# Kernel optimization log

Hardware: AMD Instinct MI355X
Metric: run time of the kernel (lower is better)

Reference implementation:

```python
import jax, jax.numpy as jnp
import numpy as np

N_FLUID = 16384
N_BND = 2048
SUPPORT = float(np.sqrt(16.0 / (np.pi * N_FLUID)))  # ~16 neighbors avg
NB = 8  # basis functions per axis (n = m = 8)
NM = NB * NB
LAYERS = [32, 64, 64, 2]
F_IN = 8
B_IN = 8


def _radius(queries, points, r):
    """numpy brute-force (chunked) radius search; rows = query idx, cols = point idx."""
    r2 = np.float32(r * r)
    pn = (points ** 2).sum(-1)
    qi_all, pj_all = [], []
    for s in range(0, queries.shape[0], 4096):
        q = queries[s:s + 4096]
        d2 = (q ** 2).sum(-1)[:, None] + pn[None, :] - 2.0 * (q @ points.T)
        qi, pj = np.nonzero(d2 < r2)
        qi_all.append(qi + s)
        pj_all.append(pj)
    return (np.concatenate(qi_all).astype(np.int32),
            np.concatenate(pj_all).astype(np.int32))


def setup_inputs() -> dict:
    rng = np.random.default_rng(0)
    fluid_pos = rng.random((N_FLUID, 2)).astype(np.float32)
    # boundary particles along the perimeter of the unit square
    t = np.linspace(0.0, 4.0, N_BND, endpoint=False).astype(np.float32)
    side = np.floor(t).astype(np.int64)
    frac = t - side
    bx = np.where(side == 0, frac, np.where(side == 1, 1.0, np.where(side == 2, 1.0 - frac, 0.0)))
    by = np.where(side == 0, 0.0, np.where(side == 1, frac, np.where(side == 2, 1.0, 1.0 - frac)))
    bnd_pos = np.stack([bx, by], -1).astype(np.float32)

    # fluid-fluid radius graph (centerIgnore: drop self edges)
    fi, fj = _radius(fluid_pos, fluid_pos, SUPPORT)
    keep = fi != fj
    f_tgt, f_src = fi[keep], fj[keep]
    # fluid(query) - boundary(source) radius graph
    b_tgt, b_src = _radius(fluid_pos, bnd_pos, SUPPORT)

    def conv_w(k, cin, cout):
        return (0.05 * rng.standard_normal((NM, cin, cout))).astype(np.float32)

    def lin_w(cin, cout):
        s = np.sqrt(6.0 / (cin + cout))
        return rng.uniform(-s, s, (cin, cout)).astype(np.float32)

    d = {
        'fluid_pos': jnp.asarray(fluid_pos),
        'bnd_pos': jnp.asarray(bnd_pos),
        'fluid_feat': jnp.asarray(rng.standard_normal((N_FLUID, F_IN)).astype(np.float32)),
        'bnd_feat': jnp.asarray(rng.standard_normal((N_BND, B_IN)).astype(np.float32)),
        'f_tgt': jnp.asarray(f_tgt), 'f_src': jnp.asarray(f_src),
        'b_tgt': jnp.asarray(b_tgt), 'b_src': jnp.asarray(b_src),
        # convs: c0 fluid->fluid (F_IN->32), c1 boundary->fluid (B_IN->32),
        #        c2 (96->64), c3 (64->64), c4 (64->2)
        'Wc0': jnp.asarray(conv_w(0, F_IN, 32)), 'bc0': jnp.zeros((32,), jnp.float32),
        'Wc1': jnp.asarray(conv_w(1, B_IN, 32)), 'bc1': jnp.zeros((32,), jnp.float32),
        'Wc2': jnp.asarray(conv_w(2, 96, 64)), 'bc2': jnp.zeros((64,), jnp.float32),
        'Wc3': jnp.asarray(conv_w(3, 64, 64)), 'bc3': jnp.zeros((64,), jnp.float32),
        'Wc4': jnp.asarray(conv_w(4, 64, 2)), 'bc4': jnp.zeros((2,), jnp.float32),
        # dense branch: l0 (F_IN->32), l1 (96->64), l2 (64->64), l3 (64->2)
        'Wl0': jnp.asarray(lin_w(F_IN, 32)), 'bl0': jnp.zeros((32,), jnp.float32),
        'Wl1': jnp.asarray(lin_w(96, 64)), 'bl1': jnp.zeros((64,), jnp.float32),
        'Wl2': jnp.asarray(lin_w(64, 64)), 'bl2': jnp.zeros((64,), jnp.float32),
        'Wl3': jnp.asarray(lin_w(64, 2)), 'bl3': jnp.zeros((2,), jnp.float32),
    }
    return d


def _hat(x, n):
    # linear 'hat' RBF basis on centers in [-1, 1]
    c = jnp.linspace(-1.0, 1.0, n, dtype=x.dtype)
    return jnp.maximum(0.0, 1.0 - jnp.abs(x[:, None] - c[None, :]) * ((n - 1) / 2.0))


def _polar(d):
    # polar coordinate mapping of normalized displacement d in [-1,1]^2
    r = jnp.sqrt(jnp.sum(d * d, -1) + 1e-12)
    theta = jnp.arctan2(d[:, 1], d[:, 0])
    return jnp.clip(jnp.stack([2.0 * r - 1.0, theta / jnp.pi], -1), -1.0, 1.0)


def _rbf_conv(x_src_nodes, src, tgt, disp, W, b, num_tgt):
    m = _polar(disp)                                   # [E,2]
    bx = _hat(m[:, 0], NB)                             # [E,n]
    by = _hat(m[:, 1], NB)                             # [E,m]
    basis = (bx[:, :, None] * by[:, None, :]).reshape(-1, NM)  # [E,nm]
    xs = x_src_nodes[src]                              # [E,cin]
    acc0 = jnp.zeros((xs.shape[0], W.shape[-1]), xs.dtype)

    def body(acc, wb):
        Wk, bk = wb
        return acc + bk[:, None] * (xs @ Wk), None

    msg, _ = jax.lax.scan(body, acc0, (W, basis.T))    # sum_k basis_k * (xs @ W_k)
    return jax.ops.segment_sum(msg, tgt, num_segments=num_tgt) + b


def reference(fluid_pos, bnd_pos, fluid_feat, bnd_feat, f_tgt, f_src, b_tgt, b_src,
              Wc0, bc0, Wc1, bc1, Wc2, bc2, Wc3, bc3, Wc4, bc4,
              Wl0, bl0, Wl1, bl1, Wl2, bl2, Wl3, bl3):
    N = fluid_feat.shape[0]
    fdisp = jnp.clip(-(fluid_pos[f_src] - fluid_pos[f_tgt]) / SUPPORT, -1.0, 1.0)
    bdisp = jnp.clip((bnd_pos[b_src] - fluid_pos[b_tgt]) / SUPPORT, -1.0, 1.0)

    lin = fluid_feat @ Wl0 + bl0
    fconv = _rbf_conv(fluid_feat, f_src, f_tgt, fdisp, Wc0, bc0, N)
    bconv = _rbf_conv(bnd_feat, b_src, b_tgt, bdisp, Wc1, bc1, N)
    ans = jnp.concatenate([lin, fconv, bconv], axis=-1)  # [N, 96]

    blocks = [(Wc2, bc2, Wl1, bl1, False), (Wc3, bc3, Wl2, bl2, True), (Wc4, bc4, Wl3, bl3, False)]
    for Wc, bc, Wl, bl, residual in blocks:
        a = jax.nn.relu(ans)
        c = _rbf_conv(a, f_src, f_tgt, fdisp, Wc, bc, N)
        dns = a @ Wl + bl
        ans = c + dns + ans if residual else c + dns
    return ans / 128.0
```

## Files before the change

kernel.cpp:

```cpp
#include <hip/hip_runtime.h>
#include <math.h>
#include <stdint.h>

#define NFL   16384
#define NCC   55
#define PADQ  128

struct EdgeData { int src; int ixiy; float fx; float fy; };

typedef _Float16 half8 __attribute__((ext_vector_type(8)));
typedef __attribute__((ext_vector_type(4))) float f32x4;

__device__ __forceinline__ float frelu(float x){ return x > 0.f ? x : 0.f; }
__device__ __forceinline__ unsigned short f2bf(float f){
    unsigned int u = __float_as_uint(f);
    unsigned int r = (u + 0x7FFFu + ((u >> 16) & 1u)) >> 16;
    return (unsigned short)r;
}

__device__ __forceinline__ EdgeData make_edge(const float* qpos, const float* ppos,
                                              int t, int s, float support, float sgn)
{
    float dx = sgn * (ppos[2*s]   - qpos[2*t])   / support;
    float dy = sgn * (ppos[2*s+1] - qpos[2*t+1]) / support;
    dx = fminf(1.f, fmaxf(-1.f, dx));
    dy = fminf(1.f, fmaxf(-1.f, dy));
    float r  = sqrtf(dx*dx + dy*dy + 1e-12f);
    float th = atan2f(dy, dx);
    float m0 = fminf(1.f, fmaxf(-1.f, 2.f*r - 1.f));
    float m1 = fminf(1.f, fmaxf(-1.f, th * 0.3183098861837907f));
    float u = (m0 + 1.f) * 3.5f;
    float v = (m1 + 1.f) * 3.5f;
    int ix = (int)u; if (ix > 6) ix = 6;
    int iy = (int)v; if (iy > 6) iy = 6;
    EdgeData ed;
    ed.src  = s;
    ed.ixiy = ix*8 + iy;
    ed.fx   = u - (float)ix;
    ed.fy   = v - (float)iy;
    return ed;
}

__global__ __launch_bounds__(256)
void setup_k(const float* __restrict__ fluid_pos, const float* __restrict__ bnd_pos,
             const int* __restrict__ f_tgt, const int* __restrict__ f_src, int nEf,
             const int* __restrict__ b_tgt, const int* __restrict__ b_src, int nEb,
             float support,
             EdgeData* __restrict__ edF, EdgeData* __restrict__ edB,
             int* __restrict__ hpart,
             int* __restrict__ rowptrF, int* __restrict__ rowptrB,
             const float* __restrict__ Wc2, const float* __restrict__ Wc3,
             const float* __restrict__ Wc0,
             _Float16* __restrict__ wt2, _Float16* __restrict__ wt3,
             unsigned short* __restrict__ wb0,
             int nA, int nB, int nC)
{
    __shared__ int lc[64];
    __shared__ _Float16 T[64][98];
    int b = blockIdx.x, tid = threadIdx.x;
    if (b < nA){
        if (tid < 64) lc[tid] = 0;
        __syncthreads();
        int e = b*256 + tid;
        if (e < nEf){
            EdgeData d = make_edge(fluid_pos, fluid_pos, f_tgt[e], f_src[e], support, -1.f);
            edF[e] = d;
            atomicAdd(&lc[d.ixiy], 1);
        }
        __syncthreads();
        if (tid < 64) hpart[b*64 + tid] = lc[tid];
    } else if (b < nA + nB){
        int e = (b - nA)*256 + tid;
        if (e < nEb)
            edB[e] = make_edge(fluid_pos, bnd_pos, b_tgt[e], b_src[e], support, 1.f);
    } else if (b < nA + nB + nC){
        int t = (b - nA - nB)*256 + tid;
        if (t > NFL) return;
        if (t == NFL){ rowptrF[NFL] = nEf; return; }
        int lo = 0, hi = nEf;
        while (lo < hi){ int mid = (lo + hi) >> 1; if (f_tgt[mid] < t) lo = mid + 1; else hi = mid; }
        rowptrF[t] = lo;
    } else if (b < nA + nB + 2*nC){
        int t = (b - nA - nB - nC)*256 + tid;
        if (t > NFL) return;
        if (t == NFL){ rowptrB[NFL] = nEb; return; }
        int lo = 0, hi = nEb;
        while (lo < hi){ int mid = (lo + hi) >> 1; if (b_tgt[mid] < t) lo = mid + 1; else hi = mid; }
        rowptrB[t] = lo;
    } else {
        int wb = b - (nA + nB + 2*nC);
        if (wb < 64){
            const float* s = Wc2 + (size_t)wb * 96 * 64;
            for (int i = tid; i < 96*64; i += 256){ int k = i/64, c = i - k*64; T[c][k] = (_Float16)s[i]; }
            __syncthreads();
            _Float16* d = wt2 + (size_t)wb * 64 * 96;
            for (int i = tid; i < 96*64; i += 256){ int c = i/96, k = i - c*96; d[i] = T[c][k]; }
        } else if (wb < 128){
            int cell = wb - 64;
            const float* s = Wc3 + (size_t)cell * 64 * 64;
            for (int i = tid; i < 64*64; i += 256){ int k = i/64, c = i - k*64; T[c][k] = (_Float16)s[i]; }
            __syncthreads();
            _Float16* d = wt3 + (size_t)cell * 64 * 64;
            for (int i = tid; i < 64*64; i += 256){ int c = i/64, k = i - c*64; d[i] = T[c][k]; }
        } else {
            for (int i = tid; i < 64*8*32; i += 256) wb0[i] = f2bf(Wc0[i]);
        }
    }
}

__global__ __launch_bounds__(1024)
void scan_pad_k(const int* __restrict__ hpart, int nHB,
                int* __restrict__ cellOff,
                int* __restrict__ gcursor, int4* __restrict__ entries)
{
    __shared__ int red[16][64];
    __shared__ int cntS[64];
    __shared__ int offS[NCC+1];
    int tid = threadIdx.x;
    int c = tid & 63, j = tid >> 6;

    int s0 = 0, s1 = 0, s2 = 0, s3 = 0;
    int b = j;
    for (; b + 48 < nHB; b += 64){
        s0 += hpart[(b     )*64 + c];
        s1 += hpart[(b + 16)*64 + c];
        s2 += hpart[(b + 32)*64 + c];
        s3 += hpart[(b + 48)*64 + c];
    }
    for (; b < nHB; b += 16) s0 += hpart[b*64 + c];
    red[j][c] = s0 + s1 + s2 + s3;
    __syncthreads();

    if (tid < 64){
        int s = 0;
#pragma unroll
        for (int k = 0; k < 16; ++k) s += red[k][tid];
        cntS[tid] = s;
        gcursor[tid] = 0;
    }
    __syncthreads();
    if (tid == 0){
        int acc = 0;
        for (int k = 0; k < NCC; ++k){
            offS[k] = acc;
            acc += ((cntS[k] + PADQ - 1) / PADQ) * PADQ;
        }
        offS[NCC] = acc;
        for (int k = 0; k <= NCC; ++k) cellOff[k] = offS[k];
    }
    __syncthreads();
    for (int k = 0; k < NCC; ++k){
        int base = offS[k] + cntS[k];
        int pads = (offS[k+1] - offS[k]) - cntS[k];
        for (int i = tid; i < pads; i += 1024)
            entries[base + i] = make_int4(0, -1, 0, 0);
    }
}

__global__ void scatter_k(const EdgeData* __restrict__ ed, int nE,
                          const int* __restrict__ cellOff,
                          int* __restrict__ gcursor,
                          int4* __restrict__ entries)
{
    __shared__ int lc[64], base[64];
    int tid = threadIdx.x;
    if (tid < 64) lc[tid] = 0;
    __syncthreads();
    int e = blockIdx.x * blockDim.x + tid;
    bool ok = e < nE;
    EdgeData d; int k = 0, r = 0;
    if (ok){ d = ed[e]; k = d.ixiy; r = atomicAdd(&lc[k], 1); }
    __syncthreads();
    if (tid < 64 && lc[tid] > 0) base[tid] = atomicAdd(&gcursor[tid], lc[tid]);
    __syncthreads();
    if (ok){
        int slot = cellOff[k] + base[k] + r;
        entries[slot] = make_int4(d.src, e, __float_as_int(d.fx), __float_as_int(d.fy));
    }
}

template<int CIN>
__global__ __launch_bounds__(256)
void conv_mfma_k(const _Float16* __restrict__ xh,
                 const int4* __restrict__ entries,
                 const int* __restrict__ cellOff,
                 const _Float16* __restrict__ wt,
                 _Float16* __restrict__ msg)
{
    constexpr int COUT = 64;
    constexpr int XROW = CIN*2 + 16;
    constexpr int C16  = CIN*2/16;
    constexpr int NK   = CIN/32;
    constexpr int NCH  = PADQ/64;

    __shared__ unsigned char XL[64 * XROW];
    __shared__ _Float16 MT[64][68];
    __shared__ float BW[4][64];
    __shared__ int   SRC[64];
    __shared__ int   EID[64];

    int total = cellOff[NCC];
    int nwg = gridDim.x, bid = blockIdx.x;
    int q = nwg >> 3, r = nwg & 7;
    int xcd = bid & 7, idx = bid >> 3;
    int swz = (xcd < r ? xcd*(q+1) : r*(q+1) + (xcd - r)*q) + idx;
    int pb = swz * PADQ;
    if (pb >= total) return;
    int tid = threadIdx.x;

    int lo_ = 0, hi_ = NCC;
    while (hi_ - lo_ > 1){ int mid = (lo_ + hi_) >> 1; if (cellOff[mid] <= pb) lo_ = mid; else hi_ = mid; }
    const int cell = lo_;
    const int kc[4] = { cell, cell+1, cell+8, cell+9 };

    const int lane = tid & 63, wv = tid >> 6;
    const int lr = lane & 15, lg = lane >> 4;
    const int cb = wv * 16;

    const _Float16* wbase = wt + (size_t)(cb + lr) * CIN + lg * 8;
    half8 bfr[4][NK];
#pragma unroll
    for (int cr = 0; cr < 4; ++cr)
#pragma unroll
        for (int kk = 0; kk < NK; ++kk)
            bfr[cr][kk] = *(const half8*)(wbase + (size_t)kc[cr]*(COUT*CIN) + kk*32);

    for (int ch = 0; ch < NCH; ++ch){
        int p0 = pb + ch * 64;

        if (tid < 64){
            int4 en = entries[p0 + tid];
            bool ok = en.y >= 0;
            float fx = __int_as_float(en.z), fy = __int_as_float(en.w);
            BW[0][tid] = ok ? (1.f-fx)*(1.f-fy) : 0.f;
            BW[1][tid] = ok ? (1.f-fx)*fy       : 0.f;
            BW[2][tid] = ok ? fx*(1.f-fy)       : 0.f;
            BW[3][tid] = ok ? fx*fy             : 0.f;
            SRC[tid] = en.x;
            EID[tid] = en.y;
        }
        __syncthreads();
        for (int i = tid; i < 64*C16; i += 256){
            int e = i / C16, c = i - e*C16;
            const uint4* sp = (const uint4*)(xh + (size_t)SRC[e]*CIN) + c;
            *(uint4*)(&XL[e*XROW + 16*c]) = *sp;
        }
        __syncthreads();

        f32x4 acc[4][4];
#pragma unroll
        for (int cr = 0; cr < 4; ++cr)
#pragma unroll
            for (int ae = 0; ae < 4; ++ae)
                acc[cr][ae] = (f32x4)0.f;

#pragma unroll
        for (int kk = 0; kk < NK; ++kk){
            half8 a[4];
#pragma unroll
            for (int ae = 0; ae < 4; ++ae)
                a[ae] = *(const half8*)(&XL[(16*ae + lr)*XROW + kk*64 + lg*16]);
#pragma unroll
            for (int cr = 0; cr < 4; ++cr)
#pragma unroll
                for (int ae = 0; ae < 4; ++ae)
                    acc[cr][ae] = __builtin_amdgcn_mfma_f32_16x16x32_f16(a[ae], bfr[cr][kk], acc[cr][ae], 0, 0, 0);
        }

#pragma unroll
        for (int ae = 0; ae < 4; ++ae){
#pragma unroll
            for (int r2 = 0; r2 < 4; ++r2){
                int E = 16*ae + lg*4 + r2;
                float v = BW[0][E]*acc[0][ae][r2] + BW[1][E]*acc[1][ae][r2]
                        + BW[2][E]*acc[2][ae][r2] + BW[3][E]*acc[3][ae][r2];
                MT[E][cb + lr] = (_Float16)v;
            }
        }
        __syncthreads();

#pragma unroll
        for (int p = 0; p < 2; ++p){
            int f = tid + p*256;
            int e = f >> 3, j = f & 7;
            int eid = EID[e];
            if (eid >= 0)
                *(uint4*)(msg + (size_t)eid*COUT + j*8) = *(const uint4*)(&MT[e][j*8]);
        }
        __syncthreads();
    }
}

template<int CIN, int COUT, int TILE_E, bool RELU>
__global__ __launch_bounds__(128)
void conv_cell_k(const float* __restrict__ x,
                 const int4* __restrict__ entries,
                 const int* __restrict__ cellOff,
                 const unsigned short* __restrict__ Wbf,
                 _Float16* __restrict__ msg)
{
    constexpr int TEP = TILE_E + 4;
    constexpr int EG  = TILE_E / 4;
    constexpr int CG  = COUT / 8;
    static_assert(EG * CG == 128, "tile/thread mismatch");
    constexpr int C4  = CIN / 4;

    __shared__ float XT[CIN][TEP];
    __shared__ unsigned short WLc[4][CIN][COUT];
    __shared__ int4 EN[TILE_E];

    int total = cellOff[NCC];
    int p0 = blockIdx.x * TILE_E;
    if (p0 >= total) return;
    int tid = threadIdx.x;

    int lo = 0, hi = NCC;
    while (hi - lo > 1){ int mid = (lo + hi) >> 1; if (cellOff[mid] <= p0) lo = mid; else hi = mid; }
    const int cell = lo;

    for (int i = tid; i < TILE_E; i += 128) EN[i] = entries[p0 + i];

    const int kc[4] = { cell, cell + 1, cell + 8, cell + 9 };
#pragma unroll
    for (int c = 0; c < 4; ++c){
        const uint4* s = (const uint4*)(Wbf + (size_t)kc[c] * (CIN * COUT));
        uint4* dlds = (uint4*)(&WLc[c][0][0]);
        for (int i = tid; i < CIN * COUT / 8; i += 128) dlds[i] = s[i];
    }
    __syncthreads();

    for (int i = tid; i < TILE_E * C4; i += 128){
        int e  = i / C4;
        int c4 = i - e * C4;
        int4 en = EN[e];
        float4 v = make_float4(0.f, 0.f, 0.f, 0.f);
        if (en.y >= 0){
            v = *(const float4*)(x + (size_t)en.x * CIN + 4 * c4);
            if (RELU){ v.x = frelu(v.x); v.y = frelu(v.y); v.z = frelu(v.z); v.w = frelu(v.w); }
        }
        XT[4*c4+0][e] = v.x;
        XT[4*c4+1][e] = v.y;
        XT[4*c4+2][e] = v.z;
        XT[4*c4+3][e] = v.w;
    }
    __syncthreads();

    const int egrp = tid % EG;
    const int cgrp = tid / EG;
    const int e0 = egrp * 4;

    float fx[4], fy[4];
    int eid[4];
#pragma unroll
    for (int j = 0; j < 4; ++j){
        int4 en = EN[e0 + j];
        fx[j] = __int_as_float(en.z);
        fy[j] = __int_as_float(en.w);
        eid[j] = en.y;
    }

    float accT[4][8];
#pragma unroll
    for (int j = 0; j < 4; ++j)
#pragma unroll
        for (int c = 0; c < 8; ++c) accT[j][c] = 0.f;

#pragma unroll
    for (int cr = 0; cr < 4; ++cr){
        float accC[4][8];
#pragma unroll
        for (int j = 0; j < 4; ++j)
#pragma unroll
            for (int c = 0; c < 8; ++c) accC[j][c] = 0.f;

#pragma unroll
        for (int ci = 0; ci < CIN; ++ci){
            float4 xv = *(const float4*)&XT[ci][e0];
            uint4 wp = *(const uint4*)&WLc[cr][ci][cgrp * 8];
            float wf0 = __uint_as_float(wp.x << 16);
            float wf1 = __uint_as_float(wp.x & 0xFFFF0000u);
            float wf2 = __uint_as_float(wp.y << 16);
            float wf3 = __uint_as_float(wp.y & 0xFFFF0000u);
            float wf4 = __uint_as_float(wp.z << 16);
            float wf5 = __uint_as_float(wp.z & 0xFFFF0000u);
            float wf6 = __uint_as_float(wp.w << 16);
            float wf7 = __uint_as_float(wp.w & 0xFFFF0000u);
            const float xe[4] = { xv.x, xv.y, xv.z, xv.w };
#pragma unroll
            for (int j = 0; j < 4; ++j){
                accC[j][0] += xe[j] * wf0;
                accC[j][1] += xe[j] * wf1;
                accC[j][2] += xe[j] * wf2;
                accC[j][3] += xe[j] * wf3;
                accC[j][4] += xe[j] * wf4;
                accC[j][5] += xe[j] * wf5;
                accC[j][6] += xe[j] * wf6;
                accC[j][7] += xe[j] * wf7;
            }
        }
#pragma unroll
        for (int j = 0; j < 4; ++j){
            float wc = (cr == 0) ? (1.f - fx[j]) * (1.f - fy[j]) :
                       (cr == 1) ? (1.f - fx[j]) * fy[j] :
                       (cr == 2) ? fx[j] * (1.f - fy[j]) :
                                   fx[j] * fy[j];
#pragma unroll
            for (int c = 0; c < 8; ++c) accT[j][c] += wc * accC[j][c];
        }
    }

#pragma unroll
    for (int j = 0; j < 4; ++j){
        if (eid[j] < 0) continue;
        half8 hv;
#pragma unroll
        for (int c = 0; c < 8; ++c) hv[c] = (_Float16)accT[j][c];
        *(half8*)(msg + (size_t)eid[j] * COUT + cgrp * 8) = hv;
    }
}

__global__ __launch_bounds__(128)
void conv2_msg_k(const _Float16* __restrict__ xh,
                 const int4* __restrict__ entries,
                 const int* __restrict__ cellOff,
                 const float* __restrict__ Wc,
                 float* __restrict__ msg2)
{
    __shared__ float WLf[4][64][2];
    int total = cellOff[NCC];
    int p0 = blockIdx.x * 128;
    if (p0 >= total) return;
    int tid = threadIdx.x;

    int lo = 0, hi = NCC;
    while (hi - lo > 1){ int mid = (lo + hi) >> 1; if (cellOff[mid] <= p0) lo = mid; else hi = mid; }
    const int cell = lo;
    const int kc[4] = { cell, cell + 1, cell + 8, cell + 9 };
#pragma unroll
    for (int c = 0; c < 4; ++c)
        ((float*)&WLf[c][0][0])[tid] = Wc[(size_t)kc[c] * 128 + tid];
    __syncthreads();

    int4 en = entries[p0 + tid];
    if (en.y < 0) return;
    float fx = __int_as_float(en.z), fy = __int_as_float(en.w);
    const _Float16* xp = xh + (size_t)en.x * 64;

    float a[4][2] = {{0.f,0.f},{0.f,0.f},{0.f,0.f},{0.f,0.f}};
#pragma unroll
    for (int ci = 0; ci < 64; ci += 8){
        half8 v = *(const half8*)(xp + ci);
#pragma unroll
        for (int j = 0; j < 8; ++j){
            float xe = (float)v[j];
#pragma unroll
            for (int cr = 0; cr < 4; ++cr){
                a[cr][0] += xe * WLf[cr][ci+j][0];
                a[cr][1] += xe * WLf[cr][ci+j][1];
            }
        }
    }
    float w0 = (1.f-fx)*(1.f-fy), w1 = (1.f-fx)*fy, w2 = fx*(1.f-fy), w3 = fx*fy;
    float m0 = w0*a[0][0] + w1*a[1][0] + w2*a[2][0] + w3*a[3][0];
    float m1 = w0*a[0][1] + w1*a[1][1] + w2*a[2][1] + w3*a[3][1];
    *(float2*)(msg2 + (size_t)en.y * 2) = make_float2(m0, m1);
}

__global__ __launch_bounds__(256)
void final_combine_k(const _Float16* __restrict__ xh,
                     const float* __restrict__ Wl3, const float* __restrict__ bl3,
                     const float* __restrict__ bc4,
                     const float* __restrict__ msg2,
                     const int* __restrict__ rowptr,
                     float* __restrict__ out)
{
    __shared__ float WS[128];
    int tid = threadIdx.x;
    if (tid < 128) WS[tid] = Wl3[tid];
    __syncthreads();

    int t = blockIdx.x * blockDim.x + tid;
    if (t >= NFL) return;
    int eb = rowptr[t], ee = rowptr[t+1];

    float a0 = bc4[0] + bl3[0];
    float a1 = bc4[1] + bl3[1];
    const _Float16* pr = xh + (size_t)t * 64;
#pragma unroll
    for (int ci = 0; ci < 64; ci += 8){
        half8 v = *(const half8*)(pr + ci);
#pragma unroll
        for (int j = 0; j < 8; ++j){
            float xe = (float)v[j];
            a0 += xe * WS[(ci+j)*2];
            a1 += xe * WS[(ci+j)*2 + 1];
        }
    }
    for (int e = eb; e < ee; ++e){
        float2 m = *(const float2*)(msg2 + (size_t)e * 2);
        a0 += m.x; a1 += m.y;
    }
    out[(size_t)t*2]     = a0 * (1.0f/128.0f);
    out[(size_t)t*2 + 1] = a1 * (1.0f/128.0f);
}

__global__ __launch_bounds__(256)
void combine0_k(const float* __restrict__ feat,
                const float* __restrict__ bnd_feat,
                const float* __restrict__ Wl0, const float* __restrict__ bl0,
                const float* __restrict__ bc0,
                const float* __restrict__ Wc1, const float* __restrict__ bc1,
                const EdgeData* __restrict__ edB,
                const int* __restrict__ rowptrB,
                const _Float16* __restrict__ msg,
                const int* __restrict__ rowptrF,
                float* __restrict__ ansA,
                _Float16* __restrict__ xbA)
{
    int t = blockIdx.x * (blockDim.x >> 6) + (threadIdx.x >> 6);
    if (t >= NFL) return;
    int lane = threadIdx.x & 63;

    if (lane < 32){
        float a = bl0[lane];
#pragma unroll
        for (int ci = 0; ci < 8; ++ci)
            a += feat[t*8 + ci] * Wl0[ci*32 + lane];
        ansA[(size_t)t*96 + lane] = a;
        xbA[(size_t)t*96 + lane]  = (_Float16)frelu(a);

        float b = bc1[lane];
        int eb = rowptrB[t], ee = rowptrB[t+1];
        for (int e = eb; e < ee; ++e){
            EdgeData d = edB[e];
            const float* xp = bnd_feat + (size_t)d.src * 8;
            const float* wp = Wc1 + (size_t)d.ixiy * 256 + lane;
            float t00 = 0.f, t01 = 0.f, t10 = 0.f, t11 = 0.f;
#pragma unroll
            for (int ci = 0; ci < 8; ++ci){
                float xv = xp[ci];
                t00 += xv * wp[ci*32];
                t01 += xv * wp[ci*32 + 256];
                t10 += xv * wp[ci*32 + 2048];
                t11 += xv * wp[ci*32 + 2304];
            }
            float wx1 = d.fx, wy1 = d.fy;
            float wx0 = 1.f - wx1, wy0 = 1.f - wy1;
            b += (wx0*wy0)*t00 + (wx0*wy1)*t01 + (wx1*wy0)*t10 + (wx1*wy1)*t11;
        }
        ansA[(size_t)t*96 + 64 + lane] = b;
        xbA[(size_t)t*96 + 64 + lane]  = (_Float16)frelu(b);
    } else {
        int c = lane - 32;
        float a = bc0[c];
        int eb = rowptrF[t], ee = rowptrF[t+1];
        for (int e = eb; e < ee; ++e)
            a += (float)msg[(size_t)e*32 + c];
        ansA[(size_t)t*96 + 32 + c] = a;
        xbA[(size_t)t*96 + 32 + c]  = (_Float16)frelu(a);
    }
}

template<int CIN, bool RESID, bool WRITE_XB>
__global__ __launch_bounds__(256)
void combine12_k(const float* __restrict__ yprev,
                 const _Float16* __restrict__ xprev,
                 const float* __restrict__ Wl, const float* __restrict__ bl,
                 const float* __restrict__ bc,
                 const _Float16* __restrict__ msg,
                 const int* __restrict__ rowptr,
                 float* __restrict__ y,
                 _Float16* __restrict__ xbnext)
{
    int t = blockIdx.x * (blockDim.x >> 6) + (threadIdx.x >> 6);
    if (t >= NFL) return;
    int lane = threadIdx.x & 63;
    int eb = rowptr[t], ee = rowptr[t+1];

    const _Float16* pr = xprev + (size_t)t * CIN;
    float acc = bc[lane] + bl[lane];
#pragma unroll 8
    for (int ci = 0; ci < CIN; ++ci)
        acc += (float)pr[ci] * Wl[ci*64 + lane];
    if (RESID) acc += yprev[(size_t)t*64 + lane];

    for (int e = eb; e < ee; ++e)
        acc += (float)msg[(size_t)e*64 + lane];
    y[(size_t)t*64 + lane] = acc;

    if (WRITE_XB)
        xbnext[(size_t)t*64 + lane] = (_Float16)frelu(acc);
}

extern "C" void kernel_launch(void* const* d_in, const int* in_sizes, int n_in,
                              void* d_out, int out_size, void* d_ws, size_t ws_size,
                              hipStream_t stream)
{
    const float* fluid_pos  = (const float*)d_in[0];
    const float* bnd_pos    = (const float*)d_in[1];
    const float* fluid_feat = (const float*)d_in[2];
    const float* bnd_feat   = (const float*)d_in[3];
    const int*   f_tgt      = (const int*)  d_in[4];
    const int*   f_src      = (const int*)  d_in[5];
    const int*   b_tgt      = (const int*)  d_in[6];
    const int*   b_src      = (const int*)  d_in[7];
    const float* Wc0 = (const float*)d_in[8];  const float* bc0 = (const float*)d_in[9];
    const float* Wc1 = (const float*)d_in[10]; const float* bc1 = (const float*)d_in[11];
    const float* Wc2 = (const float*)d_in[12]; const float* bc2 = (const float*)d_in[13];
    const float* Wc3 = (const float*)d_in[14]; const float* bc3 = (const float*)d_in[15];
    const float* Wc4 = (const float*)d_in[16]; const float* bc4 = (const float*)d_in[17];
    const float* Wl0 = (const float*)d_in[18]; const float* bl0 = (const float*)d_in[19];
    const float* Wl1 = (const float*)d_in[20]; const float* bl1 = (const float*)d_in[21];
    const float* Wl2 = (const float*)d_in[22]; const float* bl2 = (const float*)d_in[23];
    const float* Wl3 = (const float*)d_in[24]; const float* bl3 = (const float*)d_in[25];

    int nEf = in_sizes[4];
    int nEb = in_sizes[6];
    int entPadMax = nEf + NCC * PADQ;
    float support = (float)sqrt(16.0 / (M_PI * 16384.0));

    int nA = (nEf + 255)/256, nB = (nEb + 255)/256, nC = (NFL + 256)/256;

    char* w = (char*)d_ws;
    auto alloc = [&](size_t bytes){ char* r = w; w += (bytes + 255) & ~(size_t)255; return r; };
    EdgeData* edF      = (EdgeData*)alloc((size_t)nEf * sizeof(EdgeData));
    EdgeData* edB      = (EdgeData*)alloc((size_t)nEb * sizeof(EdgeData));
    int*      hpart    = (int*)     alloc((size_t)nA * 64 * sizeof(int));
    int*      cellOff  = (int*)     alloc(64 * sizeof(int));
    int*      gcursor  = (int*)     alloc(64 * sizeof(int));
    int*      rowptrF  = (int*)     alloc((NFL+1) * sizeof(int));
    int*      rowptrB  = (int*)     alloc((NFL+1) * sizeof(int));
    int4*     entries  = (int4*)    alloc((size_t)entPadMax * sizeof(int4));
    unsigned short* wb0 = (unsigned short*)alloc((size_t)64*8*32 * 2);
    _Float16* wt2      = (_Float16*)alloc((size_t)64*64*96 * 2);
    _Float16* wt3      = (_Float16*)alloc((size_t)64*64*64 * 2);
    _Float16* xbA      = (_Float16*)alloc((size_t)NFL*96 * 2);
    _Float16* xb1      = (_Float16*)alloc((size_t)NFL*64 * 2);
    _Float16* xb2      = (_Float16*)alloc((size_t)NFL*64 * 2);
    float*    ansA     = (float*)   alloc((size_t)NFL * 96 * sizeof(float));
    float*    y1       = (float*)   alloc((size_t)NFL * 64 * sizeof(float));
    float*    y2       = (float*)   alloc((size_t)NFL * 64 * sizeof(float));
    _Float16* msg      = (_Float16*)alloc((size_t)nEf * 64 * 2);
    float*    msg2     = (float*)   alloc((size_t)nEf * 2 * sizeof(float));

    setup_k<<<nA + nB + 2*nC + 129, 256, 0, stream>>>(fluid_pos, bnd_pos,
                                                      f_tgt, f_src, nEf,
                                                      b_tgt, b_src, nEb, support,
                                                      edF, edB, hpart, rowptrF, rowptrB,
                                                      Wc2, Wc3, Wc0, wt2, wt3, wb0,
                                                      nA, nB, nC);
    scan_pad_k<<<1, 1024, 0, stream>>>(hpart, nA, cellOff, gcursor, entries);
    scatter_k<<<nA, 256, 0, stream>>>(edF, nEf, cellOff, gcursor, entries);

    int gridM = (entPadMax + PADQ - 1) / PADQ;
    int gridC = (entPadMax + 127) / 128;
    dim3 tgrid(NFL/4);

    conv_cell_k<8,32,128,false><<<gridC, 128, 0, stream>>>(fluid_feat, entries, cellOff, wb0, msg);
    combine0_k<<<tgrid, 256, 0, stream>>>(fluid_feat, bnd_feat, Wl0, bl0, bc0,
                                          Wc1, bc1, edB, rowptrB,
                                          msg, rowptrF, ansA, xbA);

    conv_mfma_k<96><<<gridM, 256, 0, stream>>>(xbA, entries, cellOff, wt2, msg);
    combine12_k<96,false,true><<<tgrid, 256, 0, stream>>>(nullptr, xbA, Wl1, bl1, bc2, msg, rowptrF, y1, xb1);

    conv_mfma_k<64><<<gridM, 256, 0, stream>>>(xb1, entries, cellOff, wt3, msg);
    combine12_k<64,true,true><<<tgrid, 256, 0, stream>>>(y1, xb1, Wl2, bl2, bc3, msg, rowptrF, y2, xb2);

    conv2_msg_k<<<gridC, 128, 0, stream>>>(xb2, entries, cellOff, Wc4, msg2);
    final_combine_k<<<(NFL+255)/256, 256, 0, stream>>>(xb2, Wl3, bl3, bc4, msg2, rowptrF, (float*)d_out);
}
```

Baseline: 247.5 us.

## Fuse first fluid conv into combine0 with per-target gather from LDS weights

Removes the separate cell-tiled conv kernel for the first fluid-fluid convolution (CIN=8, COUT=32) and its fp16 message buffer round-trip. combine0 now loads the full bf16 weight bank (64x8x32) into shared memory per block and computes each target's messages directly by gathering source features per edge with bilinear weights. This saves a launch and the message write/read, but every block of 4 targets reloads 32KB of weights into LDS and does scalar per-edge math in a CSR loop.

```diff
diff --git a/kernel.cpp b/kernel.cpp
--- a/kernel.cpp
+++ b/kernel.cpp
@@ -16,6 +16,9 @@
     unsigned int u = __float_as_uint(f);
     unsigned int r = (u + 0x7FFFu + ((u >> 16) & 1u)) >> 16;
     return (unsigned short)r;
+}
+__device__ __forceinline__ float bf2f(unsigned short u){
+    return __uint_as_float(((unsigned int)u) << 16);
 }
 
 __device__ __forceinline__ EdgeData make_edge(const float* qpos, const float* ppos,
@@ -291,134 +294,6 @@
     }
 }
 
-template<int CIN, int COUT, int TILE_E, bool RELU>
-__global__ __launch_bounds__(128)
-void conv_cell_k(const float* __restrict__ x,
-                 const int4* __restrict__ entries,
-                 const int* __restrict__ cellOff,
-                 const unsigned short* __restrict__ Wbf,
-                 _Float16* __restrict__ msg)
-{
-    constexpr int TEP = TILE_E + 4;
-    constexpr int EG  = TILE_E / 4;
-    constexpr int CG  = COUT / 8;
-    static_assert(EG * CG == 128, "tile/thread mismatch");
-    constexpr int C4  = CIN / 4;
-
-    __shared__ float XT[CIN][TEP];
-    __shared__ unsigned short WLc[4][CIN][COUT];
-    __shared__ int4 EN[TILE_E];
-
-    int total = cellOff[NCC];
-    int p0 = blockIdx.x * TILE_E;
-    if (p0 >= total) return;
-    int tid = threadIdx.x;
-
-    int lo = 0, hi = NCC;
-    while (hi - lo > 1){ int mid = (lo + hi) >> 1; if (cellOff[mid] <= p0) lo = mid; else hi = mid; }
-    const int cell = lo;
-
-    for (int i = tid; i < TILE_E; i += 128) EN[i] = entries[p0 + i];
-
-    const int kc[4] = { cell, cell + 1, cell + 8, cell + 9 };
-#pragma unroll
-    for (int c = 0; c < 4; ++c){
-        const uint4* s = (const uint4*)(Wbf + (size_t)kc[c] * (CIN * COUT));
-        uint4* dlds = (uint4*)(&WLc[c][0][0]);
-        for (int i = tid; i < CIN * COUT / 8; i += 128) dlds[i] = s[i];
-    }
-    __syncthreads();
-
-    for (int i = tid; i < TILE_E * C4; i += 128){
-        int e  = i / C4;
-        int c4 = i - e * C4;
-        int4 en = EN[e];
-        float4 v = make_float4(0.f, 0.f, 0.f, 0.f);
-        if (en.y >= 0){
-            v = *(const float4*)(x + (size_t)en.x * CIN + 4 * c4);
-            if (RELU){ v.x = frelu(v.x); v.y = frelu(v.y); v.z = frelu(v.z); v.w = frelu(v.w); }
-        }
-        XT[4*c4+0][e] = v.x;
-        XT[4*c4+1][e] = v.y;
-        XT[4*c4+2][e] = v.z;
-        XT[4*c4+3][e] = v.w;
-    }
-    __syncthreads();
-
-    const int egrp = tid % EG;
-    const int cgrp = tid / EG;
-    const int e0 = egrp * 4;
-
-    float fx[4], fy[4];
-    int eid[4];
-#pragma unroll
-    for (int j = 0; j < 4; ++j){
-        int4 en = EN[e0 + j];
-        fx[j] = __int_as_float(en.z);
-        fy[j] = __int_as_float(en.w);
-        eid[j] = en.y;
-    }
-
-    float accT[4][8];
-#pragma unroll
-    for (int j = 0; j < 4; ++j)
-#pragma unroll
-        for (int c = 0; c < 8; ++c) accT[j][c] = 0.f;
-
-#pragma unroll
-    for (int cr = 0; cr < 4; ++cr){
-        float accC[4][8];
-#pragma unroll
-        for (int j = 0; j < 4; ++j)
-#pragma unroll
-            for (int c = 0; c < 8; ++c) accC[j][c] = 0.f;
-
-#pragma unroll
-        for (int ci = 0; ci < CIN; ++ci){
-            float4 xv = *(const float4*)&XT[ci][e0];
-            uint4 wp = *(const uint4*)&WLc[cr][ci][cgrp * 8];
-            float wf0 = __uint_as_float(wp.x << 16);
-            float wf1 = __uint_as_float(wp.x & 0xFFFF0000u);
-            float wf2 = __uint_as_float(wp.y << 16);
-            float wf3 = __uint_as_float(wp.y & 0xFFFF0000u);
-            float wf4 = __uint_as_float(wp.z << 16);
-            float wf5 = __uint_as_float(wp.z & 0xFFFF0000u);
-            float wf6 = __uint_as_float(wp.w << 16);
-            float wf7 = __uint_as_float(wp.w & 0xFFFF0000u);
-            const float xe[4] = { xv.x, xv.y, xv.z, xv.w };
-#pragma unroll
-            for (int j = 0; j < 4; ++j){
-                accC[j][0] += xe[j] * wf0;
-                accC[j][1] += xe[j] * wf1;
-                accC[j][2] += xe[j] * wf2;
-                accC[j][3] += xe[j] * wf3;
-                accC[j][4] += xe[j] * wf4;
-                accC[j][5] += xe[j] * wf5;
-                accC[j][6] += xe[j] * wf6;
-                accC[j][7] += xe[j] * wf7;
-            }
-        }
-#pragma unroll
-        for (int j = 0; j < 4; ++j){
-            float wc = (cr == 0) ? (1.f - fx[j]) * (1.f - fy[j]) :
-                       (cr == 1) ? (1.f - fx[j]) * fy[j] :
-                       (cr == 2) ? fx[j] * (1.f - fy[j]) :
-                                   fx[j] * fy[j];
-#pragma unroll
-            for (int c = 0; c < 8; ++c) accT[j][c] += wc * accC[j][c];
-        }
-    }
-
-#pragma unroll
-    for (int j = 0; j < 4; ++j){
-        if (eid[j] < 0) continue;
-        half8 hv;
-#pragma unroll
-        for (int c = 0; c < 8; ++c) hv[c] = (_Float16)accT[j][c];
-        *(half8*)(msg + (size_t)eid[j] * COUT + cgrp * 8) = hv;
-    }
-}
-
 __global__ __launch_bounds__(128)
 void conv2_msg_k(const _Float16* __restrict__ xh,
                  const int4* __restrict__ entries,
@@ -512,14 +387,21 @@
                 const float* __restrict__ Wc1, const float* __restrict__ bc1,
                 const EdgeData* __restrict__ edB,
                 const int* __restrict__ rowptrB,
-                const _Float16* __restrict__ msg,
+                const EdgeData* __restrict__ edF,
                 const int* __restrict__ rowptrF,
+                const unsigned short* __restrict__ wb0,
                 float* __restrict__ ansA,
                 _Float16* __restrict__ xbA)
 {
-    int t = blockIdx.x * (blockDim.x >> 6) + (threadIdx.x >> 6);
+    __shared__ unsigned short WL0[64*8*32];
+    int tid = threadIdx.x;
+    for (int i = tid; i < 64*8*32/8; i += 256)
+        ((uint4*)WL0)[i] = ((const uint4*)wb0)[i];
+    __syncthreads();
+
+    int t = blockIdx.x * 4 + (tid >> 6);
     if (t >= NFL) return;
-    int lane = threadIdx.x & 63;
+    int lane = tid & 63;
 
     if (lane < 32){
         float a = bl0[lane];
@@ -554,8 +436,23 @@
         int c = lane - 32;
         float a = bc0[c];
         int eb = rowptrF[t], ee = rowptrF[t+1];
-        for (int e = eb; e < ee; ++e)
-            a += (float)msg[(size_t)e*32 + c];
+        for (int e = eb; e < ee; ++e){
+            EdgeData d = edF[e];
+            const float* xp = feat + (size_t)d.src * 8;
+            const unsigned short* wp = WL0 + d.ixiy * 256 + c;
+            float t00 = 0.f, t01 = 0.f, t10 = 0.f, t11 = 0.f;
+#pragma unroll
+            for (int ci = 0; ci < 8; ++ci){
+                float xv = xp[ci];
+                t00 += xv * bf2f(wp[ci*32]);
+                t01 += xv * bf2f(wp[ci*32 + 256]);
+                t10 += xv * bf2f(wp[ci*32 + 2048]);
+                t11 += xv * bf2f(wp[ci*32 + 2304]);
+            }
+            float wx1 = d.fx, wy1 = d.fy;
+            float wx0 = 1.f - wx1, wy0 = 1.f - wy1;
+            a += (wx0*wy0)*t00 + (wx0*wy1)*t01 + (wx1*wy0)*t10 + (wx1*wy1)*t11;
+        }
         ansA[(size_t)t*96 + 32 + c] = a;
         xbA[(size_t)t*96 + 32 + c]  = (_Float16)frelu(a);
     }
@@ -656,10 +553,9 @@
     int gridC = (entPadMax + 127) / 128;
     dim3 tgrid(NFL/4);
 
-    conv_cell_k<8,32,128,false><<<gridC, 128, 0, stream>>>(fluid_feat, entries, cellOff, wb0, msg);
     combine0_k<<<tgrid, 256, 0, stream>>>(fluid_feat, bnd_feat, Wl0, bl0, bc0,
                                           Wc1, bc1, edB, rowptrB,
-                                          msg, rowptrF, ansA, xbA);
+                                          edF, rowptrF, wb0, ansA, xbA);
 
     conv_mfma_k<96><<<gridM, 256, 0, stream>>>(xbA, entries, cellOff, wt2, msg);
     combine12_k<96,false,true><<<tgrid, 256, 0, stream>>>(nullptr, xbA, Wl1, bl1, bc2, msg, rowptrF, y1, xb1);
```

After: 263.3 us. 6.4% more time.
